# Kernel optimization log

Measured on AMD Instinct MI355X. Metric: run time of the kernel, lower is better.

The kernel has to match this reference:

```python
import jax, jax.numpy as jnp
import numpy as np

LEAKY_SLOPE = 0.2  # LeakyReLU(0.2) attention activation from the torch module
HEADS = 4
RATES = (10, 25)


def _prod(v):
    r = 1
    for x in v:
        r *= x
    return r


def gat_conv(x_self, x_neigh, W, a_s, a_n):
    """Single GAT aggregation layer (aggregate_method='concat').
    x_self:  [..., F_in]
    x_neigh: [..., E, F_in] (leading dims reshape-compatible with x_self)
    W: [F_in, H*D], a_s/a_n: [H, D]
    Returns [..., H*D].
    """
    H = HEADS
    D = W.shape[1] // H
    lead = x_self.shape[:-1]
    E = x_neigh.shape[-2]
    z_s = (x_self @ W).reshape(lead + (H, D))                  # [..., H, D]
    z_n = (x_neigh @ W).reshape(lead + (E, H, D))              # [..., E, H, D]
    e_s = jnp.einsum('...hd,hd->...h', z_s, a_s)               # [..., H]
    e_n = jnp.einsum('...ehd,hd->...eh', z_n, a_n)             # [..., E, H]
    logits = jax.nn.leaky_relu(e_s[..., None, :] + e_n, LEAKY_SLOPE)
    alpha = jax.nn.softmax(logits, axis=-2)                    # softmax over neighbors E
    out = jnp.einsum('...eh,...ehd->...hd', alpha, z_n)        # attention-weighted sum
    return out.reshape(lead + (H * D,))


def setup_inputs() -> dict:
    key = jax.random.key(0)
    ks = jax.random.split(key, 10)
    B, F, HID, OUT = 1024, 128, 512, 256
    s = 0.05
    return {
        'h0': jax.random.normal(ks[0], (B, F), jnp.float32),
        'h1': jax.random.normal(ks[1], (B, RATES[0], F), jnp.float32),
        'h2': jax.random.normal(ks[2], (B, RATES[0] * RATES[1], F), jnp.float32),
        'W0': jax.random.normal(ks[3], (F, HID), jnp.float32) * s,
        'a0_s': jax.random.normal(ks[4], (HEADS, HID // HEADS), jnp.float32) * s,
        'a0_n': jax.random.normal(ks[5], (HEADS, HID // HEADS), jnp.float32) * s,
        'W1': jax.random.normal(ks[6], (HID, HID), jnp.float32) * s,
        'a1_s': jax.random.normal(ks[7], (HEADS, HID // HEADS), jnp.float32) * s,
        'a1_n': jax.random.normal(ks[8], (HEADS, HID // HEADS), jnp.float32) * s,
        'W_fc': jax.random.normal(ks[9], (HID, OUT), jnp.float32) * s,
    }


def reference(h0, h1, h2, W0, a0_s, a0_n, W1, a1_s, a1_n, W_fc):
    B = h0.shape[0]
    hs = [h0, h1, h2]
    layers = [(W0, a0_s, a0_n), (W1, a1_s, a1_n)]
    depth = len(RATES)
    # hierarchical sweep: layer i is applied to levels 0..depth-i-1
    for i, (W, a_s, a_n) in enumerate(layers):
        for j in range(depth - i):
            x_self = hs[j]
            x_neigh = hs[j + 1].reshape(B, _prod(RATES[:j]), RATES[j], -1)
            hs[j] = gat_conv(x_self, x_neigh, W, a_s, a_n)
    return hs[0] @ W_fc  # final Linear (no bias, no activation)
```

## Files before the change

### kernel.cpp

```cpp
#include <hip/hip_runtime.h>

__device__ __forceinline__ void gemm32(
    float* __restrict__ smem,
    const float* __restrict__ A, int lda,
    const float* __restrict__ B, int ldb,
    float* __restrict__ C, int ldc, int K,
    int m0, int col0) {
  float* As = smem;
  float* Bs = smem + 16 * 36;
  const int t = threadIdx.x;
  const int tn = t & 31, tm = t >> 5;
  const int lam = t >> 2, lak = (t & 3) * 4;
  const int lbk = t >> 4, lbn = (t & 15) * 8;
  float acc[4][4];
#pragma unroll
  for (int i = 0; i < 4; ++i)
#pragma unroll
    for (int j = 0; j < 4; ++j) acc[i][j] = 0.f;
  for (int k0 = 0; k0 < K; k0 += 16) {
    if (t < 128) {
      float4 av = *reinterpret_cast<const float4*>(A + (size_t)(m0 + lam) * lda + k0 + lak);
      As[(lak + 0) * 36 + lam] = av.x;
      As[(lak + 1) * 36 + lam] = av.y;
      As[(lak + 2) * 36 + lam] = av.z;
      As[(lak + 3) * 36 + lam] = av.w;
    }
    const float* bp = B + (size_t)(k0 + lbk) * ldb + col0 + lbn;
    float4 b0 = *reinterpret_cast<const float4*>(bp);
    float4 b1 = *reinterpret_cast<const float4*>(bp + 4);
    float* bd = &Bs[lbk * 132 + lbn];
    *reinterpret_cast<float4*>(bd) = b0;
    *reinterpret_cast<float4*>(bd + 4) = b1;
    __syncthreads();
#pragma unroll
    for (int kk = 0; kk < 16; ++kk) {
      float4 a4 = *reinterpret_cast<const float4*>(&As[kk * 36 + tm * 4]);
      float4 b4 = *reinterpret_cast<const float4*>(&Bs[kk * 132 + tn * 4]);
      float a[4] = {a4.x, a4.y, a4.z, a4.w};
      float b[4] = {b4.x, b4.y, b4.z, b4.w};
#pragma unroll
      for (int i = 0; i < 4; ++i)
#pragma unroll
        for (int j = 0; j < 4; ++j) acc[i][j] = fmaf(a[i], b[j], acc[i][j]);
    }
    __syncthreads();
  }
#pragma unroll
  for (int i = 0; i < 4; ++i) {
    float* cp = C + (size_t)(m0 + tm * 4 + i) * ldc + col0 + tn * 4;
    *reinterpret_cast<float4*>(cp) =
        make_float4(acc[i][0], acc[i][1], acc[i][2], acc[i][3]);
  }
}

template <int FIN, int TPR, int E>
__device__ __forceinline__ void gat_body(
    float* __restrict__ smem,
    const float* __restrict__ xself, const float* __restrict__ xneigh,
    const float* __restrict__ waS, const float* __restrict__ waN,
    float* __restrict__ out) {
  constexpr int MR = E + 1;
  constexpr int RPP = 256 / TPR;
  constexpr int PP = (TPR > 64) ? 8 : 4;
  float* tile = smem;
  float* partial = tile + MR * FIN;
  float* alpha = partial + MR * PP;
  const int t = threadIdx.x;
  const int el = t / TPR;
  const int f0 = (t % TPR) * 4;
  float4 wn[4], ws[4];
#pragma unroll
  for (int h = 0; h < 4; ++h) {
    wn[h] = *reinterpret_cast<const float4*>(waN + h * FIN + f0);
    ws[h] = *reinterpret_cast<const float4*>(waS + h * FIN + f0);
  }
#pragma unroll
  for (int p = 0; p * RPP < MR; ++p) {
    int e = p * RPP + el;
    if (e < MR) {
      const float* src = (e < E) ? (xneigh + (size_t)e * FIN + f0) : (xself + f0);
      float4 x = *reinterpret_cast<const float4*>(src);
      *reinterpret_cast<float4*>(tile + e * FIN + f0) = x;
      float ph[4];
#pragma unroll
      for (int h = 0; h < 4; ++h) {
        float4 w = (e < E) ? wn[h] : ws[h];
        ph[h] = x.x * w.x + x.y * w.y + x.z * w.z + x.w * w.w;
      }
#pragma unroll
      for (int h = 0; h < 4; ++h) {
        ph[h] += __shfl_xor(ph[h], 1);
        ph[h] += __shfl_xor(ph[h], 2);
        ph[h] += __shfl_xor(ph[h], 4);
        ph[h] += __shfl_xor(ph[h], 8);
        ph[h] += __shfl_xor(ph[h], 16);
        if constexpr (TPR > 64) ph[h] += __shfl_xor(ph[h], 32);
      }
      if constexpr (TPR <= 64) {
        if ((t & (TPR - 1)) == 0)
          *reinterpret_cast<float4*>(partial + e * 4) =
              make_float4(ph[0], ph[1], ph[2], ph[3]);
      } else {
        if ((t & 63) == 0) {
          int half = (t >> 6) & 1;
          *reinterpret_cast<float4*>(partial + e * 8 + half * 4) =
              make_float4(ph[0], ph[1], ph[2], ph[3]);
        }
      }
    }
  }
  __syncthreads();
  if (t < 64) {
    const int h = t & 3;
    const int e0 = t >> 2;
    float selfl = partial[E * PP + h];
    if constexpr (PP == 8) selfl += partial[E * PP + 4 + h];
    float x0 = -1e30f, x1 = -1e30f;
    if (e0 < E) {
      float v = partial[e0 * PP + h];
      if constexpr (PP == 8) v += partial[e0 * PP + 4 + h];
      float x = selfl + v;
      x0 = (x > 0.f) ? x : 0.2f * x;
    }
    if constexpr (E > 16) {
      if (e0 + 16 < E) {
        float v = partial[(e0 + 16) * PP + h];
        if constexpr (PP == 8) v += partial[(e0 + 16) * PP + 4 + h];
        float x = selfl + v;
        x1 = (x > 0.f) ? x : 0.2f * x;
      }
    }
    float m = fmaxf(x0, x1);
    m = fmaxf(m, __shfl_xor(m, 4));
    m = fmaxf(m, __shfl_xor(m, 8));
    m = fmaxf(m, __shfl_xor(m, 16));
    m = fmaxf(m, __shfl_xor(m, 32));
    float p0 = (e0 < E) ? __expf(x0 - m) : 0.f;
    float p1 = 0.f;
    if constexpr (E > 16) p1 = (e0 + 16 < E) ? __expf(x1 - m) : 0.f;
    float s = p0 + p1;
    s += __shfl_xor(s, 4);
    s += __shfl_xor(s, 8);
    s += __shfl_xor(s, 16);
    s += __shfl_xor(s, 32);
    float inv = 1.f / s;
    if (e0 < E) alpha[e0 * 4 + h] = p0 * inv;
    if constexpr (E > 16)
      if (e0 + 16 < E) alpha[(e0 + 16) * 4 + h] = p1 * inv;
  }
  __syncthreads();
  constexpr int C2 = FIN / 2;
  for (int o = t; o < 4 * C2; o += 256) {
    int h = o / C2, f = (o % C2) * 2;
    float2 acc = make_float2(0.f, 0.f);
#pragma unroll
    for (int e = 0; e < E; ++e) {
      float a = alpha[e * 4 + h];
      float2 x = *reinterpret_cast<const float2*>(tile + e * FIN + f);
      acc.x = fmaf(a, x.x, acc.x);
      acc.y = fmaf(a, x.y, acc.y);
    }
    *reinterpret_cast<float2*>(out + h * FIN + f) = acc;
  }
}

__global__ void __launch_bounds__(256) prepA(
    const float* __restrict__ W0, const float* __restrict__ a0s,
    const float* __restrict__ a0n,
    const float* __restrict__ W1, const float* __restrict__ a1s,
    const float* __restrict__ a1n, const float* __restrict__ Wfc,
    float* __restrict__ wa0s, float* __restrict__ wa0n,
    float* __restrict__ wa1s, float* __restrict__ wa1n,
    float* __restrict__ T) {
  __shared__ float smem[2688];
  const int b = blockIdx.x;
  if (b < 128) {
    int h = b >> 5, mb = (b >> 1) & 15, nb = b & 1;
    gemm32(smem, W1 + h * 128, 512, Wfc + (size_t)h * 32768, 256,
           T + (size_t)h * 131072, 256, 128, mb * 32, nb * 128);
    return;
  }
  int idx = (b - 128) * 256 + threadIdx.x;
  if (idx >= 5120) return;
  const float* W; const float* a; float* dst; int i; int FIN;
  if (idx < 512)       { W = W0; a = a0s; dst = wa0s; i = idx;        FIN = 128; }
  else if (idx < 1024) { W = W0; a = a0n; dst = wa0n; i = idx - 512;  FIN = 128; }
  else if (idx < 3072) { W = W1; a = a1s; dst = wa1s; i = idx - 1024; FIN = 512; }
  else                 { W = W1; a = a1n; dst = wa1n; i = idx - 3072; FIN = 512; }
  int f = i >> 2, h = i & 3;
  const float* wrow = W + (size_t)f * 512 + h * 128;
  const float* arow = a + h * 128;
  float v = 0.f;
#pragma unroll 8
  for (int d = 0; d < 128; ++d) v = fmaf(wrow[d], arow[d], v);
  dst[h * FIN + f] = v;
}

__global__ void __launch_bounds__(256) fusedB(
    const float* __restrict__ h0, const float* __restrict__ h1,
    const float* __restrict__ h2, const float* __restrict__ wa0s,
    const float* __restrict__ wa0n, float* __restrict__ xagg,
    const float* __restrict__ W0, const float* __restrict__ wa1s,
    const float* __restrict__ wa1n, const float* __restrict__ T,
    float* __restrict__ va1s, float* __restrict__ va1n,
    float* __restrict__ Wfinal) {
  __shared__ float smem[3532];
  const int b = blockIdx.x;
  if (b < 128) {
    int h = b >> 5, h0b = (b >> 3) & 3, mb = (b >> 1) & 3, nb = b & 1;
    gemm32(smem, W0 + h0b * 128, 512,
           T + (size_t)h * 131072 + (size_t)h0b * 32768, 256,
           Wfinal + (size_t)h * 131072 + (size_t)h0b * 32768, 256, 128,
           mb * 32, nb * 128);
    return;
  }
  if (b < 144) {
    int idx = (b - 128) * 256 + threadIdx.x;
    const float* wa = (idx < 2048) ? wa1s : wa1n;
    float* dst = (idx < 2048) ? va1s : va1n;
    int i = idx & 2047;
    int h = i >> 9, h0b = (i >> 7) & 3, f = i & 127;
    const float* w0row = W0 + (size_t)f * 512 + h0b * 128;
    const float* warow = wa + h * 512 + h0b * 128;
    float v = 0.f;
#pragma unroll 8
    for (int n = 0; n < 128; ++n) v = fmaf(w0row[n], warow[n], v);
    dst[i] = v;
    return;
  }
  if (b < 144 + 1024) {
    int n = b - 144;
    gat_body<128, 32, 10>(smem, h0 + (size_t)n * 128, h1 + (size_t)n * 1280,
                          wa0s, wa0n, xagg + (size_t)n * 512);
    return;
  }
  int g = b - 1168;
  gat_body<128, 32, 25>(smem, h1 + (size_t)g * 128, h2 + (size_t)g * 3200,
                        wa0s, wa0n, xagg + (size_t)(1024 + g) * 512);
}

__global__ void __launch_bounds__(256) gat_layer1(
    const float* __restrict__ xagg, const float* __restrict__ vaS,
    const float* __restrict__ vaN, float* __restrict__ aggx) {
  __shared__ float smem[5760];
  const int b = blockIdx.x;
  gat_body<512, 128, 10>(smem, xagg + (size_t)b * 512,
                         xagg + (size_t)(1024 + b * 10) * 512, vaS, vaN,
                         aggx + (size_t)b * 2048);
}

__global__ void __launch_bounds__(256) gemm_ksplit(
    const float* __restrict__ A, const float* __restrict__ B,
    float* __restrict__ Cpart) {
  __shared__ float smem[2688];
  const int ks = blockIdx.z;
  gemm32(smem, A + ks * 256, 2048, B + (size_t)ks * 65536, 256,
         Cpart + (size_t)ks * 262144, 256, 256, blockIdx.x * 32,
         blockIdx.y * 128);
}

__global__ void __launch_bounds__(256) reduce8(
    const float* __restrict__ Cpart, float* __restrict__ out) {
  int i = blockIdx.x * 256 + threadIdx.x;
  const float4* p = reinterpret_cast<const float4*>(Cpart) + i;
  float4 s = p[0];
#pragma unroll
  for (int ks = 1; ks < 8; ++ks) {
    float4 v = p[(size_t)ks * 65536];
    s.x += v.x; s.y += v.y; s.z += v.z; s.w += v.w;
  }
  reinterpret_cast<float4*>(out)[i] = s;
}

extern "C" void kernel_launch(void* const* d_in, const int* in_sizes, int n_in,
                              void* d_out, int out_size, void* d_ws, size_t ws_size,
                              hipStream_t stream) {
  const float* h0  = (const float*)d_in[0];
  const float* h1  = (const float*)d_in[1];
  const float* h2  = (const float*)d_in[2];
  const float* W0  = (const float*)d_in[3];
  const float* a0s = (const float*)d_in[4];
  const float* a0n = (const float*)d_in[5];
  const float* W1  = (const float*)d_in[6];
  const float* a1s = (const float*)d_in[7];
  const float* a1n = (const float*)d_in[8];
  const float* Wfc = (const float*)d_in[9];
  float* out = (float*)d_out;

  float* ws = (float*)d_ws;
  float* wa0s   = ws;
  float* wa0n   = wa0s + 512;
  float* wa1s   = wa0n + 512;
  float* wa1n   = wa1s + 2048;
  float* va1s   = wa1n + 2048;
  float* va1n   = va1s + 2048;
  float* T      = va1n + 2048;
  float* Wfinal = T + 524288;
  float* xaggA  = Wfinal + 524288;
  float* aggx   = xaggA + 11264 * 512;
  float* Cpart  = aggx + 2097152;

  prepA<<<148, 256, 0, stream>>>(W0, a0s, a0n, W1, a1s, a1n, Wfc,
                                 wa0s, wa0n, wa1s, wa1n, T);
  fusedB<<<11408, 256, 0, stream>>>(h0, h1, h2, wa0s, wa0n, xaggA,
                                    W0, wa1s, wa1n, T, va1s, va1n, Wfinal);
  gat_layer1<<<1024, 256, 0, stream>>>(xaggA, va1s, va1n, aggx);
  gemm_ksplit<<<dim3(32, 2, 8), 256, 0, stream>>>(aggx, Wfinal, Cpart);
  reduce8<<<256, 256, 0, stream>>>(Cpart, out);
}
```

Before: 263.7 us.

## Fuse all stages into one persistent kernel with software grid barriers

Replaces the five kernel launches with a single persistent kernel of 512 blocks that loops over the former work items and synchronises stages with atomic-counter grid barriers. The GAT body also gets a transposed alpha layout held in registers, a butterfly shuffle reduction that reduces all four heads at once, and a per-thread four-head accumulation for the 512-wide layer. The aim is to remove launch gaps and tail effects between stages. In exchange it assumes all 512 blocks are co-resident (two per CU), adds a memset, and can serialise some work behind the barriers.

New measurement: 495.2 us. +87.8%, slower.

```diff
diff --git a/kernel.cpp b/kernel.cpp
--- a/kernel.cpp
+++ b/kernel.cpp
@@ -1,4 +1,18 @@
 #include <hip/hip_runtime.h>
+
+#define GRID 512
+
+__device__ __forceinline__ void grid_bar(unsigned* bar, int which) {
+  __syncthreads();
+  if (threadIdx.x == 0) {
+    __threadfence();
+    unsigned* c = bar + which * 16;
+    atomicAdd(c, 1u);
+    while (atomicAdd(c, 0u) < (unsigned)GRID) __builtin_amdgcn_s_sleep(2);
+    __threadfence();
+  }
+  __syncthreads();
+}
 
 __device__ __forceinline__ void gemm32(
     float* __restrict__ smem,
@@ -62,9 +76,10 @@
   constexpr int MR = E + 1;
   constexpr int RPP = 256 / TPR;
   constexpr int PP = (TPR > 64) ? 8 : 4;
+  constexpr int EP = 32;
   float* tile = smem;
   float* partial = tile + MR * FIN;
-  float* alpha = partial + MR * PP;
+  float* alphaT = partial + MR * PP;
   const int t = threadIdx.x;
   const int el = t / TPR;
   const int f0 = (t % TPR) * 4;
@@ -87,25 +102,24 @@
         float4 w = (e < E) ? wn[h] : ws[h];
         ph[h] = x.x * w.x + x.y * w.y + x.z * w.z + x.w * w.w;
       }
-#pragma unroll
-      for (int h = 0; h < 4; ++h) {
-        ph[h] += __shfl_xor(ph[h], 1);
-        ph[h] += __shfl_xor(ph[h], 2);
-        ph[h] += __shfl_xor(ph[h], 4);
-        ph[h] += __shfl_xor(ph[h], 8);
-        ph[h] += __shfl_xor(ph[h], 16);
-        if constexpr (TPR > 64) ph[h] += __shfl_xor(ph[h], 32);
-      }
-      if constexpr (TPR <= 64) {
-        if ((t & (TPR - 1)) == 0)
-          *reinterpret_cast<float4*>(partial + e * 4) =
-              make_float4(ph[0], ph[1], ph[2], ph[3]);
+      const int b0 = t & 1, b1 = (t >> 1) & 1;
+      float m0 = b0 ? ph[1] : ph[0];
+      float o0 = b0 ? ph[0] : ph[1];
+      float m1 = b0 ? ph[3] : ph[2];
+      float o1 = b0 ? ph[2] : ph[3];
+      m0 += __shfl_xor(o0, 1);
+      m1 += __shfl_xor(o1, 1);
+      float mk = b1 ? m1 : m0;
+      float gv = b1 ? m0 : m1;
+      mk += __shfl_xor(gv, 2);
+      mk += __shfl_xor(mk, 4);
+      mk += __shfl_xor(mk, 8);
+      mk += __shfl_xor(mk, 16);
+      if constexpr (TPR > 64) {
+        mk += __shfl_xor(mk, 32);
+        if ((t & 63) < 4) partial[e * 8 + ((t >> 6) & 1) * 4 + (t & 3)] = mk;
       } else {
-        if ((t & 63) == 0) {
-          int half = (t >> 6) & 1;
-          *reinterpret_cast<float4*>(partial + e * 8 + half * 4) =
-              make_float4(ph[0], ph[1], ph[2], ph[3]);
-        }
+        if ((t & (TPR - 1)) < 4) partial[e * 4 + (t & 3)] = mk;
       }
     }
   }
@@ -144,132 +158,157 @@
     s += __shfl_xor(s, 16);
     s += __shfl_xor(s, 32);
     float inv = 1.f / s;
-    if (e0 < E) alpha[e0 * 4 + h] = p0 * inv;
+    if (e0 < E) alphaT[h * EP + e0] = p0 * inv;
     if constexpr (E > 16)
-      if (e0 + 16 < E) alpha[(e0 + 16) * 4 + h] = p1 * inv;
+      if (e0 + 16 < E) alphaT[h * EP + e0 + 16] = p1 * inv;
   }
   __syncthreads();
-  constexpr int C2 = FIN / 2;
-  for (int o = t; o < 4 * C2; o += 256) {
-    int h = o / C2, f = (o % C2) * 2;
+  constexpr int NQ = (E + 3) / 4;
+  if constexpr (FIN == 128) {
+    const int h = t >> 6, f = (t & 63) * 2;
+    float al[NQ * 4];
+#pragma unroll
+    for (int q = 0; q < NQ; ++q)
+      *reinterpret_cast<float4*>(&al[q * 4]) =
+          *reinterpret_cast<const float4*>(&alphaT[h * EP + q * 4]);
     float2 acc = make_float2(0.f, 0.f);
 #pragma unroll
     for (int e = 0; e < E; ++e) {
-      float a = alpha[e * 4 + h];
       float2 x = *reinterpret_cast<const float2*>(tile + e * FIN + f);
-      acc.x = fmaf(a, x.x, acc.x);
-      acc.y = fmaf(a, x.y, acc.y);
+      acc.x = fmaf(al[e], x.x, acc.x);
+      acc.y = fmaf(al[e], x.y, acc.y);
     }
     *reinterpret_cast<float2*>(out + h * FIN + f) = acc;
-  }
-}
-
-__global__ void __launch_bounds__(256) prepA(
-    const float* __restrict__ W0, const float* __restrict__ a0s,
-    const float* __restrict__ a0n,
+  } else {
+    const int f = t * 2;
+    float al[4][NQ * 4];
+#pragma unroll
+    for (int h = 0; h < 4; ++h)
+#pragma unroll
+      for (int q = 0; q < NQ; ++q)
+        *reinterpret_cast<float4*>(&al[h][q * 4]) =
+            *reinterpret_cast<const float4*>(&alphaT[h * EP + q * 4]);
+    float2 acc[4];
+#pragma unroll
+    for (int h = 0; h < 4; ++h) acc[h] = make_float2(0.f, 0.f);
+#pragma unroll
+    for (int e = 0; e < E; ++e) {
+      float2 x = *reinterpret_cast<const float2*>(tile + e * FIN + f);
+#pragma unroll
+      for (int h = 0; h < 4; ++h) {
+        acc[h].x = fmaf(al[h][e], x.x, acc[h].x);
+        acc[h].y = fmaf(al[h][e], x.y, acc[h].y);
+      }
+    }
+#pragma unroll
+    for (int h = 0; h < 4; ++h)
+      *reinterpret_cast<float2*>(out + h * FIN + f) = acc[h];
+  }
+}
+
+__global__ void __launch_bounds__(256, 2) gat_fused(
+    const float* __restrict__ h0, const float* __restrict__ h1,
+    const float* __restrict__ h2, const float* __restrict__ W0,
+    const float* __restrict__ a0s, const float* __restrict__ a0n,
     const float* __restrict__ W1, const float* __restrict__ a1s,
     const float* __restrict__ a1n, const float* __restrict__ Wfc,
-    float* __restrict__ wa0s, float* __restrict__ wa0n,
-    float* __restrict__ wa1s, float* __restrict__ wa1n,
-    float* __restrict__ T) {
-  __shared__ float smem[2688];
-  const int b = blockIdx.x;
-  if (b < 128) {
-    int h = b >> 5, mb = (b >> 1) & 15, nb = b & 1;
+    float* __restrict__ wsb, float* __restrict__ out,
+    unsigned* __restrict__ bar) {
+  __shared__ float smem[5848];
+  const int bid = blockIdx.x;
+  const int t = threadIdx.x;
+
+  float* wa0s = wsb;
+  float* wa0n = wa0s + 512;
+  float* wa1s = wa0n + 512;
+  float* wa1n = wa1s + 2048;
+  float* va1s = wa1n + 2048;
+  float* va1n = va1s + 2048;
+  float* T = va1n + 2048;
+  float* Wfinal = T + 524288;
+  float* xagg = Wfinal + 524288;
+  float* aggx = xagg + 5767168;
+  float* Cpart = xagg;
+
+  if (bid < 128) {
+    int h = bid >> 5, mb = (bid >> 1) & 15, nb = bid & 1;
     gemm32(smem, W1 + h * 128, 512, Wfc + (size_t)h * 32768, 256,
            T + (size_t)h * 131072, 256, 128, mb * 32, nb * 128);
-    return;
-  }
-  int idx = (b - 128) * 256 + threadIdx.x;
-  if (idx >= 5120) return;
-  const float* W; const float* a; float* dst; int i; int FIN;
-  if (idx < 512)       { W = W0; a = a0s; dst = wa0s; i = idx;        FIN = 128; }
-  else if (idx < 1024) { W = W0; a = a0n; dst = wa0n; i = idx - 512;  FIN = 128; }
-  else if (idx < 3072) { W = W1; a = a1s; dst = wa1s; i = idx - 1024; FIN = 512; }
-  else                 { W = W1; a = a1n; dst = wa1n; i = idx - 3072; FIN = 512; }
-  int f = i >> 2, h = i & 3;
-  const float* wrow = W + (size_t)f * 512 + h * 128;
-  const float* arow = a + h * 128;
-  float v = 0.f;
-#pragma unroll 8
-  for (int d = 0; d < 128; ++d) v = fmaf(wrow[d], arow[d], v);
-  dst[h * FIN + f] = v;
-}
-
-__global__ void __launch_bounds__(256) fusedB(
-    const float* __restrict__ h0, const float* __restrict__ h1,
-    const float* __restrict__ h2, const float* __restrict__ wa0s,
-    const float* __restrict__ wa0n, float* __restrict__ xagg,
-    const float* __restrict__ W0, const float* __restrict__ wa1s,
-    const float* __restrict__ wa1n, const float* __restrict__ T,
-    float* __restrict__ va1s, float* __restrict__ va1n,
-    float* __restrict__ Wfinal) {
-  __shared__ float smem[3532];
-  const int b = blockIdx.x;
-  if (b < 128) {
-    int h = b >> 5, h0b = (b >> 3) & 3, mb = (b >> 1) & 3, nb = b & 1;
-    gemm32(smem, W0 + h0b * 128, 512,
-           T + (size_t)h * 131072 + (size_t)h0b * 32768, 256,
-           Wfinal + (size_t)h * 131072 + (size_t)h0b * 32768, 256, 128,
-           mb * 32, nb * 128);
-    return;
-  }
-  if (b < 144) {
-    int idx = (b - 128) * 256 + threadIdx.x;
-    const float* wa = (idx < 2048) ? wa1s : wa1n;
-    float* dst = (idx < 2048) ? va1s : va1n;
-    int i = idx & 2047;
-    int h = i >> 9, h0b = (i >> 7) & 3, f = i & 127;
-    const float* w0row = W0 + (size_t)f * 512 + h0b * 128;
-    const float* warow = wa + h * 512 + h0b * 128;
+  } else if (bid < 148) {
+    int idx = (bid - 128) * 256 + t;
+    const float* W; const float* a; float* dst; int i; int FINW;
+    if (idx < 512)       { W = W0; a = a0s; dst = wa0s; i = idx;        FINW = 128; }
+    else if (idx < 1024) { W = W0; a = a0n; dst = wa0n; i = idx - 512;  FINW = 128; }
+    else if (idx < 3072) { W = W1; a = a1s; dst = wa1s; i = idx - 1024; FINW = 512; }
+    else                 { W = W1; a = a1n; dst = wa1n; i = idx - 3072; FINW = 512; }
+    int f = i >> 2, hh = i & 3;
+    const float* wrow = W + (size_t)f * 512 + hh * 128;
+    const float* arow = a + hh * 128;
     float v = 0.f;
 #pragma unroll 8
-    for (int n = 0; n < 128; ++n) v = fmaf(w0row[n], warow[n], v);
-    dst[i] = v;
-    return;
-  }
-  if (b < 144 + 1024) {
-    int n = b - 144;
-    gat_body<128, 32, 10>(smem, h0 + (size_t)n * 128, h1 + (size_t)n * 1280,
-                          wa0s, wa0n, xagg + (size_t)n * 512);
-    return;
-  }
-  int g = b - 1168;
-  gat_body<128, 32, 25>(smem, h1 + (size_t)g * 128, h2 + (size_t)g * 3200,
-                        wa0s, wa0n, xagg + (size_t)(1024 + g) * 512);
-}
-
-__global__ void __launch_bounds__(256) gat_layer1(
-    const float* __restrict__ xagg, const float* __restrict__ vaS,
-    const float* __restrict__ vaN, float* __restrict__ aggx) {
-  __shared__ float smem[5760];
-  const int b = blockIdx.x;
-  gat_body<512, 128, 10>(smem, xagg + (size_t)b * 512,
-                         xagg + (size_t)(1024 + b * 10) * 512, vaS, vaN,
-                         aggx + (size_t)b * 2048);
-}
-
-__global__ void __launch_bounds__(256) gemm_ksplit(
-    const float* __restrict__ A, const float* __restrict__ B,
-    float* __restrict__ Cpart) {
-  __shared__ float smem[2688];
-  const int ks = blockIdx.z;
-  gemm32(smem, A + ks * 256, 2048, B + (size_t)ks * 65536, 256,
-         Cpart + (size_t)ks * 262144, 256, 256, blockIdx.x * 32,
-         blockIdx.y * 128);
-}
-
-__global__ void __launch_bounds__(256) reduce8(
-    const float* __restrict__ Cpart, float* __restrict__ out) {
-  int i = blockIdx.x * 256 + threadIdx.x;
-  const float4* p = reinterpret_cast<const float4*>(Cpart) + i;
-  float4 s = p[0];
-#pragma unroll
-  for (int ks = 1; ks < 8; ++ks) {
-    float4 v = p[(size_t)ks * 65536];
-    s.x += v.x; s.y += v.y; s.z += v.z; s.w += v.w;
-  }
-  reinterpret_cast<float4*>(out)[i] = s;
+    for (int d = 0; d < 128; ++d) v = fmaf(wrow[d], arow[d], v);
+    dst[hh * FINW + f] = v;
+  }
+  grid_bar(bar, 0);
+
+  for (int i = bid; i < 11408; i += GRID) {
+    if (i < 128) {
+      int h = i >> 5, h0b = (i >> 3) & 3, mb = (i >> 1) & 3, nb = i & 1;
+      gemm32(smem, W0 + h0b * 128, 512,
+             T + (size_t)h * 131072 + (size_t)h0b * 32768, 256,
+             Wfinal + (size_t)h * 131072 + (size_t)h0b * 32768, 256, 128,
+             mb * 32, nb * 128);
+    } else if (i < 144) {
+      int idx = (i - 128) * 256 + t;
+      const float* wa = (idx < 2048) ? wa1s : wa1n;
+      float* dst = (idx < 2048) ? va1s : va1n;
+      int j = idx & 2047;
+      int hh = j >> 9, h0b = (j >> 7) & 3, f = j & 127;
+      const float* w0row = W0 + (size_t)f * 512 + h0b * 128;
+      const float* warow = wa + hh * 512 + h0b * 128;
+      float v = 0.f;
+#pragma unroll 8
+      for (int n = 0; n < 128; ++n) v = fmaf(w0row[n], warow[n], v);
+      dst[j] = v;
+    } else if (i < 144 + 10240) {
+      int g = i - 144;
+      gat_body<128, 32, 25>(smem, h1 + (size_t)g * 128, h2 + (size_t)g * 3200,
+                            wa0s, wa0n, xagg + (size_t)(1024 + g) * 512);
+    } else {
+      int n = i - 10384;
+      gat_body<128, 32, 10>(smem, h0 + (size_t)n * 128, h1 + (size_t)n * 1280,
+                            wa0s, wa0n, xagg + (size_t)n * 512);
+    }
+    __syncthreads();
+  }
+  grid_bar(bar, 1);
+
+  for (int ii = bid; ii < 1024; ii += GRID) {
+    gat_body<512, 128, 10>(smem, xagg + (size_t)ii * 512,
+                           xagg + (size_t)(1024 + ii * 10) * 512, va1s, va1n,
+                           aggx + (size_t)ii * 2048);
+    __syncthreads();
+  }
+  grid_bar(bar, 2);
+
+  {
+    int ks = bid >> 6, mb = (bid >> 1) & 31, nb = bid & 1;
+    gemm32(smem, aggx + ks * 256, 2048, Wfinal + (size_t)ks * 65536, 256,
+           Cpart + (size_t)ks * 262144, 256, 256, mb * 32, nb * 128);
+  }
+  grid_bar(bar, 3);
+
+  if (t < 128) {
+    int i = (bid << 7) + t;
+    const float4* p = reinterpret_cast<const float4*>(Cpart) + i;
+    float4 s = p[0];
+#pragma unroll
+    for (int ks = 1; ks < 8; ++ks) {
+      float4 v = p[(size_t)ks * 65536];
+      s.x += v.x; s.y += v.y; s.z += v.z; s.w += v.w;
+    }
+    reinterpret_cast<float4*>(out)[i] = s;
+  }
 }
 
 extern "C" void kernel_launch(void* const* d_in, const int* in_sizes, int n_in,
@@ -285,26 +324,10 @@
   const float* a1s = (const float*)d_in[7];
   const float* a1n = (const float*)d_in[8];
   const float* Wfc = (const float*)d_in[9];
-  float* out = (float*)d_out;
 
   float* ws = (float*)d_ws;
-  float* wa0s   = ws;
-  float* wa0n   = wa0s + 512;
-  float* wa1s   = wa0n + 512;
-  float* wa1n   = wa1s + 2048;
-  float* va1s   = wa1n + 2048;
-  float* va1n   = va1s + 2048;
-  float* T      = va1n + 2048;
-  float* Wfinal = T + 524288;
-  float* xaggA  = Wfinal + 524288;
-  float* aggx   = xaggA + 11264 * 512;
-  float* Cpart  = aggx + 2097152;
-
-  prepA<<<148, 256, 0, stream>>>(W0, a0s, a0n, W1, a1s, a1n, Wfc,
-                                 wa0s, wa0n, wa1s, wa1n, T);
-  fusedB<<<11408, 256, 0, stream>>>(h0, h1, h2, wa0s, wa0n, xaggA,
-                                    W0, wa1s, wa1n, T, va1s, va1n, Wfinal);
-  gat_layer1<<<1024, 256, 0, stream>>>(xaggA, va1s, va1n, aggx);
-  gemm_ksplit<<<dim3(32, 2, 8), 256, 0, stream>>>(aggx, Wfinal, Cpart);
-  reduce8<<<256, 256, 0, stream>>>(Cpart, out);
-}
+  unsigned* bar = (unsigned*)(ws + 8922112);
+  hipMemsetAsync(bar, 0, 256, stream);
+  gat_fused<<<GRID, 256, 0, stream>>>(h0, h1, h2, W0, a0s, a0n, W1, a1s, a1n,
+                                      Wfc, ws, (float*)d_out, bar);
+}
```
